# Kernel optimization log

Measured on AMD Instinct MI355X. Metric: run time of the kernel, lower is better.

## Reference

```python
import jax, jax.numpy as jnp
import numpy as np

V, E, H = 32000, 512, 1024  # vocab, embed_dim, hidden_dim
B, S = 32, 64
PAD = 0


def _init(key, shape, fan_in):
    return jax.random.normal(key, shape, jnp.float32) * (1.0 / np.sqrt(fan_in))


def setup_inputs() -> dict:
    key = jax.random.key(0)
    ks = jax.random.split(key, 16)
    tok_embed = _init(ks[0], (V, E), E).at[PAD].set(0.0)  # padding_idx row zeroed
    inp = {
        "image_emb": jax.random.normal(ks[1], (B, E), jnp.float32),
        "retrieved_emb": jax.random.normal(ks[2], (B, E), jnp.float32),
        "tokens_in": jax.random.randint(ks[3], (B, S), 0, V, jnp.int64),
        "tok_embed": tok_embed,
        "init_h_W": _init(ks[4], (H, E), E),
        "init_h_b": jnp.zeros((H,), jnp.float32),
        "gru_W_ih": _init(ks[5], (3 * H, 2 * E), 2 * E),
        "gru_W_hh": _init(ks[6], (3 * H, H), H),
        "gru_b_ih": jnp.zeros((3 * H,), jnp.float32),
        "gru_b_hh": jnp.zeros((3 * H,), jnp.float32),
        "gate_W": _init(ks[7], (1, H + 2 * E), H + 2 * E),
        "gate_b": jnp.zeros((1,), jnp.float32),
        "out_W": _init(ks[8], (V, H), H),
        "out_b": jnp.zeros((V,), jnp.float32),
    }
    return inp


def _gru_cell(x, h, W_ih, W_hh, b_ih, b_hh):
    # PyTorch GRU cell math
    gi = x @ W_ih.T + b_ih  # [B, 3H]
    gh = h @ W_hh.T + b_hh
    i_r, i_z, i_n = jnp.split(gi, 3, axis=-1)
    h_r, h_z, h_n = jnp.split(gh, 3, axis=-1)
    r = jax.nn.sigmoid(i_r + h_r)
    z = jax.nn.sigmoid(i_z + h_z)
    n = jnp.tanh(i_n + r * h_n)
    return (1.0 - z) * n + z * h


def reference(image_emb, retrieved_emb, tokens_in, tok_embed, init_h_W, init_h_b,
              gru_W_ih, gru_W_hh, gru_b_ih, gru_b_hh, gate_W, gate_b, out_W, out_b):
    tok = tok_embed[tokens_in]  # [B, S, E]
    h0 = jnp.tanh(image_emb @ init_h_W.T + init_h_b)  # [B, H]

    def step(h, x_t):
        gate_in = jnp.concatenate([h, image_emb, retrieved_emb], axis=-1)  # [B, H+2E]
        alpha = jax.nn.sigmoid(gate_in @ gate_W.T + gate_b)  # [B, 1]
        fused = alpha * image_emb + (1.0 - alpha) * retrieved_emb  # [B, E]
        gru_in = jnp.concatenate([x_t, fused], axis=-1)  # [B, 2E]
        h_new = _gru_cell(gru_in, h, gru_W_ih, gru_W_hh, gru_b_ih, gru_b_hh)
        logit = h_new @ out_W.T + out_b  # [B, V]
        return h_new, logit

    _, logits = jax.lax.scan(step, h0, jnp.swapaxes(tok, 0, 1))  # [S, B, V]
    return jnp.swapaxes(logits, 0, 1)  # [B, S, V]
```

## Files before the change

kernel.cpp:

```cpp
#include <hip/hip_runtime.h>
#include <hip/hip_bf16.h>
#include <stdint.h>

#define B_ 32
#define S_ 64
#define E_ 512
#define H_ 1024
#define V_ 32000
#define H3_ 3072
#define NPROD 64
#define NCONS 192
#define NGRID (NPROD + NCONS)
#define NPANEL 250
#define NJOBS (NPANEL * 16)

typedef __bf16 bf16x8 __attribute__((ext_vector_type(8)));
typedef float f32x4 __attribute__((ext_vector_type(4)));
using bf16 = __hip_bfloat16;

__device__ __forceinline__ unsigned short f2bf(float f) {
  __hip_bfloat16 h = __float2bfloat16(f);
  return __builtin_bit_cast(unsigned short, h);
}
__device__ __forceinline__ float bf2f(unsigned short u) {
  return __bfloat162float(__builtin_bit_cast(__hip_bfloat16, u));
}

__device__ __forceinline__ void async16(void* lds, const void* g) {
  __builtin_amdgcn_global_load_lds(
      (const __attribute__((address_space(1))) unsigned int*)g,
      (__attribute__((address_space(3))) unsigned int*)lds, 16, 0, 0);
}

__device__ __forceinline__ void st_u32(unsigned* p, unsigned v) {
  __hip_atomic_store(p, v, __ATOMIC_RELAXED, __HIP_MEMORY_SCOPE_AGENT);
}
__device__ __forceinline__ unsigned ld_u32(const unsigned* p) {
  return __hip_atomic_load(p, __ATOMIC_RELAXED, __HIP_MEMORY_SCOPE_AGENT);
}
__device__ __forceinline__ f32x4 ld16_mall(const void* p) {
  f32x4 r;
  asm volatile("global_load_dwordx4 %0, %1, off sc0 sc1" : "=v"(r) : "v"(p));
  return r;
}

__device__ __forceinline__ int hswz(int b, int ig) {
  return ((((b >> 4) * 32 + (ig >> 5)) * 64) + ((b & 15) + (((ig >> 3) & 3) << 4))) * 8 + (ig & 7);
}


__global__ void gather_tok(const int* __restrict__ toks, const float* __restrict__ emb,
                           bf16* __restrict__ Abf) {
  int m = blockIdx.x;
  int b = m & 31, t = m >> 5;
  int token = toks[b * S_ + t];
  const float* src = emb + (size_t)token * E_;
  bf16* dst = Abf + (size_t)m * E_;
  int k = threadIdx.x * 4;
  f32x4 v = *(const f32x4*)(src + k);
  dst[k + 0] = __float2bfloat16(v[0]);
  dst[k + 1] = __float2bfloat16(v[1]);
  dst[k + 2] = __float2bfloat16(v[2]);
  dst[k + 3] = __float2bfloat16(v[3]);
}

__global__ void cvt_wihx(const float* __restrict__ Wih, bf16* __restrict__ Wx) {
  int j = blockIdx.x;
  int k = threadIdx.x * 4;
  f32x4 v = *(const f32x4*)(Wih + (size_t)j * 1024 + k);
  bf16* d = Wx + (size_t)j * 512 + k;
  d[0] = __float2bfloat16(v[0]);
  d[1] = __float2bfloat16(v[1]);
  d[2] = __float2bfloat16(v[2]);
  d[3] = __float2bfloat16(v[3]);
}

__global__ __launch_bounds__(256) void prep_kernel(
    const bf16* __restrict__ Abf, const bf16* __restrict__ Wihx, float* __restrict__ gix,
    const float* __restrict__ img, const float* __restrict__ retr,
    const float* __restrict__ ihW, const float* __restrict__ ihb,
    const float* __restrict__ Wih, const float* __restrict__ gW,
    const float* __restrict__ gb, const float* __restrict__ outW,
    ushort* __restrict__ Wb, float* __restrict__ h32, bf16* __restrict__ hbf0,
    float* __restrict__ u, float* __restrict__ v, float* __restrict__ cg) {
  __shared__ __align__(16) char psm[66048];
  int bid = blockIdx.x, tid = threadIdx.x;

  if (bid < 384) {
    const int nb = 384, mtiles = 16;
    bf16* Ald = (bf16*)psm;
    bf16* Bld = (bf16*)(psm + 8192);
    int swz = (bid & 7) * (nb >> 3) + (bid >> 3);
    int tm = swz % mtiles, tn = swz / mtiles;
    int l = tid & 63, w = tid >> 6;
    const int K = 512, N = H3_;
    const bf16* ga = Abf + (size_t)(tm * 128 + w * 16 + (l >> 2)) * K + (l & 3) * 8;
    const bf16* gbp = Wihx + (size_t)(tn * 128 + w * 16 + (l >> 2)) * K + (l & 3) * 8;
    char* lA = (char*)Ald + w * 1024;
    char* lB = (char*)Bld + w * 1024;
    f32x4 acc[4][4] = {};
    int wm = (w >> 1) * 64, wn = (w & 1) * 64;
    int lr = l & 15, lk = (l >> 4) * 8;
    for (int kt = 0; kt < K; kt += 32) {
      async16(lA, ga);
      async16(lA + 4096, ga + (size_t)64 * K);
      async16(lB, gbp);
      async16(lB + 4096, gbp + (size_t)64 * K);
      ga += 32; gbp += 32;
      __syncthreads();
      bf16x8 af[4], bfv[4];
#pragma unroll
      for (int mi = 0; mi < 4; ++mi) af[mi] = *(const bf16x8*)&Ald[(wm + mi * 16 + lr) * 32 + lk];
#pragma unroll
      for (int ni = 0; ni < 4; ++ni) bfv[ni] = *(const bf16x8*)&Bld[(wn + ni * 16 + lr) * 32 + lk];
#pragma unroll
      for (int mi = 0; mi < 4; ++mi)
#pragma unroll
        for (int ni = 0; ni < 4; ++ni)
          acc[mi][ni] = __builtin_amdgcn_mfma_f32_16x16x32_bf16(af[mi], bfv[ni], acc[mi][ni], 0, 0, 0);
      __syncthreads();
    }
    int cr = (l >> 4) * 4, cc = l & 15;
#pragma unroll
    for (int mi = 0; mi < 4; ++mi)
#pragma unroll
      for (int ni = 0; ni < 4; ++ni) {
        int col = tn * 128 + wn + ni * 16 + cc;
#pragma unroll
        for (int rr = 0; rr < 4; ++rr) {
          int row = tm * 128 + wm + mi * 16 + cr + rr;
          gix[(size_t)row * N + col] = acc[mi][ni][rr];
        }
      }

  } else if (bid < 1152) {
    int local = bid - 384;
    bool isU = local < 384;
    const float* src = isU ? img : retr;
    float* dst = isU ? u : v;
    int j0 = (isU ? local : local - 384) * 8;
    float(*sim)[E_ + 1] = (float(*)[E_ + 1])psm;
    for (int i = tid; i < B_ * E_ / 4; i += 256) {
      f32x4 vv = ((const f32x4*)src)[i];
      int r = (i * 4) / E_, c = (i * 4) % E_;
      sim[r][c + 0] = vv[0]; sim[r][c + 1] = vv[1]; sim[r][c + 2] = vv[2]; sim[r][c + 3] = vv[3];
    }
    __syncthreads();
    int b = tid & 31;
    int j = j0 + (tid >> 5);
    const float* wr = Wih + (size_t)j * 1024 + 512;
    float acc = 0.f;
    for (int k = 0; k < E_; k += 4) {
      f32x4 w4 = *(const f32x4*)(wr + k);
      acc += w4[0] * sim[b][k] + w4[1] * sim[b][k + 1] + w4[2] * sim[b][k + 2] + w4[3] * sim[b][k + 3];
    }
    dst[b * H3_ + j] = acc;

  } else if (bid < 1280) {
    int local = bid - 1152;
    float(*sim)[E_ + 1] = (float(*)[E_ + 1])psm;
    for (int i = tid; i < B_ * E_ / 4; i += 256) {
      f32x4 vv = ((const f32x4*)img)[i];
      int r = (i * 4) / E_, c = (i * 4) % E_;
      sim[r][c + 0] = vv[0]; sim[r][c + 1] = vv[1]; sim[r][c + 2] = vv[2]; sim[r][c + 3] = vv[3];
    }
    __syncthreads();
    int b = tid & 31, il = tid >> 5;
    int i = local * 8 + il;
    const float* wr = ihW + (size_t)i * E_;
    float acc = 0.f;
    for (int k = 0; k < E_; k += 4) {
      f32x4 w4 = *(const f32x4*)(wr + k);
      acc += w4[0] * sim[b][k] + w4[1] * sim[b][k + 1] + w4[2] * sim[b][k + 2] + w4[3] * sim[b][k + 3];
    }
    float hv = tanhf(acc + ihb[i]);
    h32[b * H_ + i] = hv;
    hbf0[hswz(b, i)] = __float2bfloat16(hv);

  } else if (bid < 1312) {
    int b = bid - 1280;
    float* red = (float*)psm;
    float acc = 0.f;
    for (int k = tid; k < E_; k += 256)
      acc += img[b * E_ + k] * gW[1024 + k] + retr[b * E_ + k] * gW[1536 + k];
    red[tid] = acc;
    __syncthreads();
    for (int s = 128; s > 0; s >>= 1) {
      if (tid < s) red[tid] += red[tid + s];
      __syncthreads();
    }
    if (tid == 0) cg[b] = red[0] + gb[0];

  } else {
    long n4 = (long)V_ * H_ / 4;
    long stride = 1024L * 256;
    for (long i = (long)(bid - 1312) * 256 + tid; i < n4; i += stride) {
      f32x4 vv = *(const f32x4*)(outW + i * 4);
      ushort4 o;
      o.x = f2bf(vv[0]); o.y = f2bf(vv[1]); o.z = f2bf(vv[2]); o.w = f2bf(vv[3]);
      ((ushort4*)Wb)[i] = o;
    }
  }
}

__device__ __forceinline__ void step_sync(unsigned* flags, int bi, unsigned val) {
  __syncthreads();
  if (threadIdx.x == 0) st_u32(flags + bi * 32, val);
  if (threadIdx.x < NPROD) {
    const unsigned* f = flags + threadIdx.x * 32;
    while (ld_u32(f) < val) __builtin_amdgcn_s_sleep(1);
  }
  __syncthreads();
}

__global__ __launch_bounds__(256, 1) void fused_persist(
    const float* __restrict__ Whh, const float* __restrict__ gixAll,
    const float* __restrict__ u, const float* __restrict__ v,
    const float* __restrict__ cg, const float* __restrict__ gW,
    const float* __restrict__ bih, const float* __restrict__ bhh,
    const float* __restrict__ h32init, bf16* __restrict__ hbf,
    unsigned* __restrict__ flags, const bf16* __restrict__ Wb,
    const float* __restrict__ outb, float* __restrict__ out) {
  __shared__ __align__(16) char smem[32768];
  int bi = blockIdx.x;
  int tid = threadIdx.x;

  if (bi < NPROD) {
    int w = tid >> 6, l = tid & 63;
    int lr = l & 15, lk8 = (l >> 4) * 8;
    int kbase = w * 256;
    float(*red)[4][2][64][4] = (float(*)[4][2][64][4])smem;

    bf16x8 whi[3][8], wlo[3][8];
#pragma unroll
    for (int g = 0; g < 3; ++g)
#pragma unroll
      for (int ks = 0; ks < 8; ++ks) {
        const float* wp = Whh + (size_t)(g * H_ + bi * 16 + lr) * H_ + kbase + ks * 32 + lk8;
        f32x4 a0 = *(const f32x4*)wp;
        f32x4 a1 = *(const f32x4*)(wp + 4);
        bf16x8 h8, l8;
#pragma unroll
        for (int jj = 0; jj < 4; ++jj) {
          unsigned short hb0 = f2bf(a0[jj]);
          unsigned short hb1 = f2bf(a1[jj]);
          h8[jj] = __builtin_bit_cast(__bf16, hb0);
          h8[jj + 4] = __builtin_bit_cast(__bf16, hb1);
          l8[jj] = __builtin_bit_cast(__bf16, f2bf(a0[jj] - bf2f(hb0)));
          l8[jj + 4] = __builtin_bit_cast(__bf16, f2bf(a1[jj] - bf2f(hb1)));
        }
        whi[g][ks] = h8;
        wlo[g][ks] = l8;
      }
    bf16x8 gwf[8];
#pragma unroll
    for (int ks = 0; ks < 8; ++ks) {
      int kk = (w * 8 + ks) * 32 + (l >> 4) * 8;
      f32x4 g0 = *(const f32x4*)(gW + kk);
      f32x4 g1 = *(const f32x4*)(gW + kk + 4);
      bf16x8 gf;
#pragma unroll
      for (int jj = 0; jj < 4; ++jj) {
        gf[jj] = __builtin_bit_cast(__bf16, f2bf(g0[jj]));
        gf[jj + 4] = __builtin_bit_cast(__bf16, f2bf(g1[jj]));
      }
      gwf[ks] = gf;
    }

    int bq = tid >> 3;
    int il0 = (tid & 7) * 2;
    float uq[2][3], vq[2][3], biq[2][3], bhq[2][3], hold[2];
    float cgq = cg[bq];
#pragma unroll
    for (int q = 0; q < 2; ++q) {
      int ig = bi * 16 + il0 + q;
#pragma unroll
      for (int g = 0; g < 3; ++g) {
        uq[q][g] = u[bq * H3_ + g * H_ + ig];
        vq[q][g] = v[bq * H3_ + g * H_ + ig];
        biq[q][g] = bih[g * H_ + ig];
        bhq[q][g] = bhh[g * H_ + ig];
      }
      hold[q] = h32init[bq * H_ + ig];
    }
    int btq = bq >> 4, breg = bq & 3, lrow = ((bq & 15) >> 2) * 16;

    for (int t = 0; t < S_; ++t) {
      const char* hb = (const char*)hbf + (size_t)t * 65536;
      bf16x8 hh_all[2][8];
#pragma unroll
      for (int bt = 0; bt < 2; ++bt)
#pragma unroll
        for (int ks = 0; ks < 8; ++ks) {
          int off = ((bt * 32 + w * 8 + ks) * 64 + l) * 16;
          hh_all[bt][ks] = __builtin_bit_cast(bf16x8, ld16_mall(hb + off));
        }
      float gxv[2][3];
      {
        const float* gx = gixAll + ((size_t)t * B_ + bq) * H3_;
#pragma unroll
        for (int q = 0; q < 2; ++q) {
          int ig = bi * 16 + il0 + q;
          gxv[q][0] = gx[ig];
          gxv[q][1] = gx[H_ + ig];
          gxv[q][2] = gx[2 * H_ + ig];
        }
      }
      asm volatile("s_waitcnt vmcnt(0)" ::: "memory");
      __builtin_amdgcn_sched_barrier(0);

      f32x4 acc[4][2] = {};
#pragma unroll
      for (int ks = 0; ks < 8; ++ks) {
#pragma unroll
        for (int bt = 0; bt < 2; ++bt) {
          bf16x8 hh = hh_all[bt][ks];
          acc[0][bt] = __builtin_amdgcn_mfma_f32_16x16x32_bf16(hh, whi[0][ks], acc[0][bt], 0, 0, 0);
          acc[0][bt] = __builtin_amdgcn_mfma_f32_16x16x32_bf16(hh, wlo[0][ks], acc[0][bt], 0, 0, 0);
          acc[1][bt] = __builtin_amdgcn_mfma_f32_16x16x32_bf16(hh, whi[1][ks], acc[1][bt], 0, 0, 0);
          acc[1][bt] = __builtin_amdgcn_mfma_f32_16x16x32_bf16(hh, wlo[1][ks], acc[1][bt], 0, 0, 0);
          acc[2][bt] = __builtin_amdgcn_mfma_f32_16x16x32_bf16(hh, whi[2][ks], acc[2][bt], 0, 0, 0);
          acc[2][bt] = __builtin_amdgcn_mfma_f32_16x16x32_bf16(hh, wlo[2][ks], acc[2][bt], 0, 0, 0);
          acc[3][bt] = __builtin_amdgcn_mfma_f32_16x16x32_bf16(hh, gwf[ks], acc[3][bt], 0, 0, 0);
        }
      }
#pragma unroll
      for (int g = 0; g < 4; ++g)
#pragma unroll
        for (int bt = 0; bt < 2; ++bt)
          *(f32x4*)&red[w][g][bt][l][0] = acc[g][bt];
      __syncthreads();

      int lane0 = lrow + il0;
      float ad = red[0][3][btq][lane0][breg] + red[1][3][btq][lane0][breg] +
                 red[2][3][btq][lane0][breg] + red[3][3][btq][lane0][breg];
      float a = 1.f / (1.f + expf(-(ad + cgq)));
      unsigned short h16[2];
#pragma unroll
      for (int q = 0; q < 2; ++q) {
        int lane = lrow + il0 + q;
        float sr = red[0][0][btq][lane][breg] + red[1][0][btq][lane][breg] +
                   red[2][0][btq][lane][breg] + red[3][0][btq][lane][breg];
        float sz = red[0][1][btq][lane][breg] + red[1][1][btq][lane][breg] +
                   red[2][1][btq][lane][breg] + red[3][1][btq][lane][breg];
        float sn = red[0][2][btq][lane][breg] + red[1][2][btq][lane][breg] +
                   red[2][2][btq][lane][breg] + red[3][2][btq][lane][breg];
        float ir = gxv[q][0] + a * uq[q][0] + (1.f - a) * vq[q][0] + biq[q][0];
        float iz = gxv[q][1] + a * uq[q][1] + (1.f - a) * vq[q][1] + biq[q][1];
        float in_ = gxv[q][2] + a * uq[q][2] + (1.f - a) * vq[q][2] + biq[q][2];
        float r = 1.f / (1.f + expf(-(ir + sr + bhq[q][0])));
        float z = 1.f / (1.f + expf(-(iz + sz + bhq[q][1])));
        float nn = tanhf(in_ + r * (sn + bhq[q][2]));
        float hv = (1.f - z) * nn + z * hold[q];
        hold[q] = hv;
        h16[q] = f2bf(hv);
      }
      {
        unsigned hipack = (unsigned)h16[0] | ((unsigned)h16[1] << 16);
        int off = hswz(bq, bi * 16 + il0);
        unsigned* hi32 = (unsigned*)hbf + (size_t)(t + 1) * 16384;
        st_u32(hi32 + (off >> 1), hipack);
      }
      if (t < S_ - 1) step_sync(flags, bi, t + 1);
    }
    __syncthreads();
    if (tid == 0) st_u32(flags + bi * 32, S_);

  } else {
    int c = bi - NPROD;
    int l = tid & 63, w = tid >> 6;
    int wm = (w >> 1) * 64, wn = (w & 1) * 64;
    int lr = l & 15, lk = (l >> 4) * 8;
    bf16* Bld = (bf16*)smem;
    const char* hb_base = (const char*)hbf;

    for (int j = c; j < NJOBS; j += NCONS) {
      int batch = j / NPANEL;
      int panel = j - batch * NPANEL;
      int s0 = batch * 4 + 1;
      unsigned need = (unsigned)(batch * 4 + 4);
      if (w == 0) {
        const unsigned* f = flags + l * 32;
        while (ld_u32(f) < need) __builtin_amdgcn_s_sleep(16);
      }
      __builtin_amdgcn_sched_barrier(0);
      __builtin_amdgcn_s_barrier();
      __builtin_amdgcn_sched_barrier(0);

      const bf16* gb = Wb + (size_t)(panel * 128 + w * 16 + (l >> 2)) * 1024 + (l & 3) * 8;
      f32x4 acc[4][4] = {};
      bf16x8 afr[2][4];
#pragma unroll
      for (int mi = 0; mi < 4; ++mi) {
        int r16 = (wm >> 4) + mi;
        const char* pa = hb_base + (size_t)(s0 + (r16 >> 1)) * 65536 +
                         (((r16 & 1) * 32 + 0) * 64 + l) * 16;
        afr[0][mi] = __builtin_bit_cast(bf16x8, ld16_mall(pa));
      }
#pragma unroll
      for (int kt = 0; kt < 32; ++kt) {
        char* lB = smem + (kt & 1) * 8192 + w * 1024;
        async16(lB, gb);
        async16(lB + 4096, gb + (size_t)64 * 1024);
        gb += 32;
        if (kt < 31) {
#pragma unroll
          for (int mi = 0; mi < 4; ++mi) {
            int r16 = (wm >> 4) + mi;
            const char* pa = hb_base + (size_t)(s0 + (r16 >> 1)) * 65536 +
                             (((r16 & 1) * 32 + (kt + 1)) * 64 + l) * 16;
            afr[(kt + 1) & 1][mi] = __builtin_bit_cast(bf16x8, ld16_mall(pa));
          }
          asm volatile("s_waitcnt vmcnt(4)" ::: "memory");
        } else {
          asm volatile("s_waitcnt vmcnt(0)" ::: "memory");
        }
        __builtin_amdgcn_sched_barrier(0);
        __builtin_amdgcn_s_barrier();
        __builtin_amdgcn_sched_barrier(0);
        const bf16* Bh = Bld + (kt & 1) * 4096;
        bf16x8 bfv[4];
#pragma unroll
        for (int ni = 0; ni < 4; ++ni)
          bfv[ni] = *(const bf16x8*)&Bh[(wn + ni * 16 + lr) * 32 + lk];
#pragma unroll
        for (int mi = 0; mi < 4; ++mi)
#pragma unroll
          for (int ni = 0; ni < 4; ++ni)
            acc[mi][ni] = __builtin_amdgcn_mfma_f32_16x16x32_bf16(afr[kt & 1][mi], bfv[ni],
                                                                  acc[mi][ni], 0, 0, 0);
      }
      int cr = (l >> 4) * 4, cc = l & 15;
#pragma unroll
      for (int mi = 0; mi < 4; ++mi)
#pragma unroll
        for (int ni = 0; ni < 4; ++ni) {
          int col = panel * 128 + wn + ni * 16 + cc;
          float bv = outb[col];
#pragma unroll
          for (int rr = 0; rr < 4; ++rr) {
            int gr = wm + mi * 16 + cr + rr;
            int t = s0 - 1 + (gr >> 5);
            int b = gr & 31;
            out[(size_t)(b * S_ + t) * V_ + col] = acc[mi][ni][rr] + bv;
          }
        }
    }
  }
}

extern "C" void kernel_launch(void* const* d_in, const int* in_sizes, int n_in, void* d_out,
                              int out_size, void* d_ws, size_t ws_size, hipStream_t stream) {
  const float* img  = (const float*)d_in[0];
  const float* retr = (const float*)d_in[1];
  const int*   toks = (const int*)d_in[2];
  const float* temb = (const float*)d_in[3];
  const float* ihW  = (const float*)d_in[4];
  const float* ihb  = (const float*)d_in[5];
  const float* Wih  = (const float*)d_in[6];
  const float* Whh  = (const float*)d_in[7];
  const float* bih  = (const float*)d_in[8];
  const float* bhh  = (const float*)d_in[9];
  const float* gW   = (const float*)d_in[10];
  const float* gb   = (const float*)d_in[11];
  const float* outW = (const float*)d_in[12];
  const float* outb = (const float*)d_in[13];
  float* out = (float*)d_out;

  char* ws = (char*)d_ws;
  bf16* Wb     = (bf16*)ws;  ws += (size_t)V_ * H_ * 2;
  float* gix   = (float*)ws; ws += (size_t)S_ * B_ * H3_ * 4;
  bf16* Wihx   = (bf16*)ws;  ws += (size_t)H3_ * E_ * 2;
  bf16* Abf    = (bf16*)ws;  ws += (size_t)B_ * S_ * E_ * 2;
  float* u     = (float*)ws; ws += (size_t)B_ * H3_ * 4;
  float* v     = (float*)ws; ws += (size_t)B_ * H3_ * 4;
  float* h32i  = (float*)ws; ws += (size_t)B_ * H_ * 4;
  bf16* hbf    = (bf16*)ws;  ws += (size_t)(S_ + 1) * B_ * H_ * 2;
  float* cg    = (float*)ws; ws += 128;
  unsigned* flags = (unsigned*)ws; ws += NPROD * 32 * 4;

  gather_tok<<<B_ * S_, 128, 0, stream>>>(toks, temb, Abf);
  cvt_wihx<<<H3_, 128, 0, stream>>>(Wih, Wihx);
  (void)hipMemsetAsync(flags, 0, NPROD * 32 * 4, stream);

  prep_kernel<<<2336, 256, 0, stream>>>(Abf, Wihx, gix, img, retr, ihW, ihb, Wih, gW, gb,
                                        outW, (ushort*)Wb, h32i, hbf, u, v, cg);

  fused_persist<<<NGRID, 256, 0, stream>>>(Whh, gix, u, v, cg, gW, bih, bhh, h32i,
                                           hbf, flags, Wb, outb, out);
}
```

Before: 448.6 us.

## Double consumer M-tile to 8 timesteps per job and prefetch producer gate inputs

Consumer blocks now cover 8 timesteps (256 rows) per vocab panel instead of 4, so each out_W panel streamed from memory is reused across twice as many rows and total weight traffic is halved. This doubles accumulator and A-fragment registers and makes consumers wait for more recurrence steps before starting. Producers also prefetch the next step's input-gate projections before the step sync, taking that load off the critical recurrent path.

```diff
diff --git a/kernel.cpp b/kernel.cpp
--- a/kernel.cpp
+++ b/kernel.cpp
@@ -12,7 +12,8 @@
 #define NCONS 192
 #define NGRID (NPROD + NCONS)
 #define NPANEL 250
-#define NJOBS (NPANEL * 16)
+#define NGROUP 8
+#define NJOBS (NPANEL * NGROUP)
 
 typedef __bf16 bf16x8 __attribute__((ext_vector_type(8)));
 typedef float f32x4 __attribute__((ext_vector_type(4)));
@@ -285,6 +286,18 @@
     }
     int btq = bq >> 4, breg = bq & 3, lrow = ((bq & 15) >> 2) * 16;
 
+    float gxn[2][3];
+    {
+      const float* gx = gixAll + (size_t)bq * H3_;
+#pragma unroll
+      for (int q = 0; q < 2; ++q) {
+        int ig = bi * 16 + il0 + q;
+        gxn[q][0] = gx[ig];
+        gxn[q][1] = gx[H_ + ig];
+        gxn[q][2] = gx[2 * H_ + ig];
+      }
+    }
+
     for (int t = 0; t < S_; ++t) {
       const char* hb = (const char*)hbf + (size_t)t * 65536;
       bf16x8 hh_all[2][8];
@@ -296,15 +309,9 @@
           hh_all[bt][ks] = __builtin_bit_cast(bf16x8, ld16_mall(hb + off));
         }
       float gxv[2][3];
-      {
-        const float* gx = gixAll + ((size_t)t * B_ + bq) * H3_;
-#pragma unroll
-        for (int q = 0; q < 2; ++q) {
-          int ig = bi * 16 + il0 + q;
-          gxv[q][0] = gx[ig];
-          gxv[q][1] = gx[H_ + ig];
-          gxv[q][2] = gx[2 * H_ + ig];
-        }
+#pragma unroll
+      for (int q = 0; q < 2; ++q) {
+        gxv[q][0] = gxn[q][0]; gxv[q][1] = gxn[q][1]; gxv[q][2] = gxn[q][2];
       }
       asm volatile("s_waitcnt vmcnt(0)" ::: "memory");
       __builtin_amdgcn_sched_barrier(0);
@@ -361,7 +368,17 @@
         unsigned* hi32 = (unsigned*)hbf + (size_t)(t + 1) * 16384;
         st_u32(hi32 + (off >> 1), hipack);
       }
-      if (t < S_ - 1) step_sync(flags, bi, t + 1);
+      if (t < S_ - 1) {
+        const float* gx = gixAll + ((size_t)(t + 1) * B_ + bq) * H3_;
+#pragma unroll
+        for (int q = 0; q < 2; ++q) {
+          int ig = bi * 16 + il0 + q;
+          gxn[q][0] = gx[ig];
+          gxn[q][1] = gx[H_ + ig];
+          gxn[q][2] = gx[2 * H_ + ig];
+        }
+        step_sync(flags, bi, t + 1);
+      }
     }
     __syncthreads();
     if (tid == 0) st_u32(flags + bi * 32, S_);
@@ -375,10 +392,10 @@
     const char* hb_base = (const char*)hbf;
 
     for (int j = c; j < NJOBS; j += NCONS) {
-      int batch = j / NPANEL;
-      int panel = j - batch * NPANEL;
-      int s0 = batch * 4 + 1;
-      unsigned need = (unsigned)(batch * 4 + 4);
+      int group = j / NPANEL;
+      int panel = j - group * NPANEL;
+      int s0 = group * 8 + 1;
+      unsigned need = (unsigned)(group * 8 + 8);
       if (w == 0) {
         const unsigned* f = flags + l * 32;
         while (ld_u32(f) < need) __builtin_amdgcn_s_sleep(16);
@@ -388,15 +405,17 @@
       __builtin_amdgcn_sched_barrier(0);
 
       const bf16* gb = Wb + (size_t)(panel * 128 + w * 16 + (l >> 2)) * 1024 + (l & 3) * 8;
-      f32x4 acc[4][4] = {};
-      bf16x8 afr[2][4];
-#pragma unroll
-      for (int mi = 0; mi < 4; ++mi) {
-        int r16 = (wm >> 4) + mi;
-        const char* pa = hb_base + (size_t)(s0 + (r16 >> 1)) * 65536 +
-                         (((r16 & 1) * 32 + 0) * 64 + l) * 16;
-        afr[0][mi] = __builtin_bit_cast(bf16x8, ld16_mall(pa));
-      }
+      f32x4 acc[2][4][4] = {};
+      bf16x8 afr[2][2][4];
+#pragma unroll
+      for (int mt = 0; mt < 2; ++mt)
+#pragma unroll
+        for (int mi = 0; mi < 4; ++mi) {
+          int r16 = mt * 8 + (wm >> 4) + mi;
+          const char* pa = hb_base + (size_t)(s0 + (r16 >> 1)) * 65536 +
+                           (((r16 & 1) * 32 + 0) * 64 + l) * 16;
+          afr[0][mt][mi] = __builtin_bit_cast(bf16x8, ld16_mall(pa));
+        }
 #pragma unroll
       for (int kt = 0; kt < 32; ++kt) {
         char* lB = smem + (kt & 1) * 8192 + w * 1024;
@@ -405,13 +424,15 @@
         gb += 32;
         if (kt < 31) {
 #pragma unroll
-          for (int mi = 0; mi < 4; ++mi) {
-            int r16 = (wm >> 4) + mi;
-            const char* pa = hb_base + (size_t)(s0 + (r16 >> 1)) * 65536 +
-                             (((r16 & 1) * 32 + (kt + 1)) * 64 + l) * 16;
-            afr[(kt + 1) & 1][mi] = __builtin_bit_cast(bf16x8, ld16_mall(pa));
-          }
-          asm volatile("s_waitcnt vmcnt(4)" ::: "memory");
+          for (int mt = 0; mt < 2; ++mt)
+#pragma unroll
+            for (int mi = 0; mi < 4; ++mi) {
+              int r16 = mt * 8 + (wm >> 4) + mi;
+              const char* pa = hb_base + (size_t)(s0 + (r16 >> 1)) * 65536 +
+                               (((r16 & 1) * 32 + (kt + 1)) * 64 + l) * 16;
+              afr[(kt + 1) & 1][mt][mi] = __builtin_bit_cast(bf16x8, ld16_mall(pa));
+            }
+          asm volatile("s_waitcnt vmcnt(8)" ::: "memory");
         } else {
           asm volatile("s_waitcnt vmcnt(0)" ::: "memory");
         }
@@ -424,27 +445,31 @@
         for (int ni = 0; ni < 4; ++ni)
           bfv[ni] = *(const bf16x8*)&Bh[(wn + ni * 16 + lr) * 32 + lk];
 #pragma unroll
+        for (int mt = 0; mt < 2; ++mt)
+#pragma unroll
+          for (int mi = 0; mi < 4; ++mi)
+#pragma unroll
+            for (int ni = 0; ni < 4; ++ni)
+              acc[mt][mi][ni] = __builtin_amdgcn_mfma_f32_16x16x32_bf16(afr[kt & 1][mt][mi], bfv[ni],
+                                                                        acc[mt][mi][ni], 0, 0, 0);
+      }
+      int cr = (l >> 4) * 4, cc = l & 15;
+#pragma unroll
+      for (int mt = 0; mt < 2; ++mt)
+#pragma unroll
         for (int mi = 0; mi < 4; ++mi)
 #pragma unroll
-          for (int ni = 0; ni < 4; ++ni)
-            acc[mi][ni] = __builtin_amdgcn_mfma_f32_16x16x32_bf16(afr[kt & 1][mi], bfv[ni],
-                                                                  acc[mi][ni], 0, 0, 0);
-      }
-      int cr = (l >> 4) * 4, cc = l & 15;
-#pragma unroll
-      for (int mi = 0; mi < 4; ++mi)
-#pragma unroll
-        for (int ni = 0; ni < 4; ++ni) {
-          int col = panel * 128 + wn + ni * 16 + cc;
-          float bv = outb[col];
-#pragma unroll
-          for (int rr = 0; rr < 4; ++rr) {
-            int gr = wm + mi * 16 + cr + rr;
-            int t = s0 - 1 + (gr >> 5);
-            int b = gr & 31;
-            out[(size_t)(b * S_ + t) * V_ + col] = acc[mi][ni][rr] + bv;
+          for (int ni = 0; ni < 4; ++ni) {
+            int col = panel * 128 + wn + ni * 16 + cc;
+            float bv = outb[col];
+#pragma unroll
+            for (int rr = 0; rr < 4; ++rr) {
+              int gr = mt * 128 + wm + mi * 16 + cr + rr;
+              int t = group * 8 + (gr >> 5);
+              int b = gr & 31;
+              out[(size_t)(b * S_ + t) * V_ + col] = acc[mt][mi][ni][rr] + bv;
+            }
           }
-        }
     }
   }
 }
```

Result: faster. 417.3 us (-7.0%).
